# Performance work log

Measured on AMD Instinct MI355X. Metric: run time of the kernel, lower is better.

## Reference

```python
import jax, jax.numpy as jnp
import numpy as np


def setup_inputs() -> dict:
    key = jax.random.key(0)
    ks = jax.random.split(key, 10)
    N, E, F = 20000, 320000, 128
    q = jax.random.normal(ks[0], (N, F), dtype=jnp.float32)
    mu = jax.random.normal(ks[1], (N, 3, F), dtype=jnp.float32)
    W_ij = jax.random.normal(ks[2], (E, 3 * F), dtype=jnp.float32)
    dir_ij = jax.random.normal(ks[3], (E, 3), dtype=jnp.float32)
    # unit displacement vectors
    dir_ij = dir_ij / jnp.linalg.norm(dir_ij, axis=-1, keepdims=True)
    W1 = jax.random.normal(ks[4], (F, F), dtype=jnp.float32) * (1.0 / np.sqrt(F))
    b1 = jax.random.normal(ks[5], (F,), dtype=jnp.float32) * 0.01
    W2 = jax.random.normal(ks[6], (F, 3 * F), dtype=jnp.float32) * (1.0 / np.sqrt(F))
    b2 = jax.random.normal(ks[7], (3 * F,), dtype=jnp.float32) * 0.01
    idx_i = jax.random.randint(ks[8], (E,), 0, N, dtype=jnp.int64 if jax.config.jax_enable_x64 else jnp.int32)
    idx_j = jax.random.randint(ks[9], (E,), 0, N, dtype=jnp.int64 if jax.config.jax_enable_x64 else jnp.int32)
    return {"q": q, "mu": mu, "W_ij": W_ij, "dir_ij": dir_ij,
            "W1": W1, "b1": b1, "W2": W2, "b2": b2,
            "idx_i": idx_i, "idx_j": idx_j, "n_atoms": N}


def reference(q, mu, W_ij, dir_ij, W1, b1, W2, b2, idx_i, idx_j, n_atoms):
    Fdim = q.shape[-1]
    # context_net: Linear(F,F) -> SiLU -> Linear(F,3F), computed per node [N,3F]
    ctx = jax.nn.silu(q @ W1 + b1) @ W2 + b2
    # gather by source node, elementwise filter: [E,3F]
    x = W_ij * ctx[idx_j]
    dq, dmu_r, dmu_mu = jnp.split(x, 3, axis=-1)  # each [E,F]
    # scatter-add scalar messages to nodes [N,F]
    dq = jax.ops.segment_sum(dq, idx_i, num_segments=n_atoms)
    # vector messages: [E,3,F]
    dmu = dmu_r[:, None, :] * dir_ij[:, :, None] + dmu_mu[:, None, :] * mu[idx_j]
    dmu = jax.ops.segment_sum(dmu, idx_i, num_segments=n_atoms)
    return (q + dq, mu + dmu)
```

## Files before the change

kernel.cpp:

```cpp
#include <hip/hip_runtime.h>


static __host__ __device__ inline size_t ws_align(size_t x) { return (x + 255) & ~(size_t)255; }

template <bool SILU>
__global__ __launch_bounds__(256, 2) void gemm_bias_act_kernel(
    const float* __restrict__ A, const float* __restrict__ B,
    const float* __restrict__ bias, float* __restrict__ C,
    int M, int Ncols)
{
    __shared__ float As[128][68];
    __shared__ float Bs[128][68];

    const int t    = threadIdx.x;
    const int row0 = blockIdx.x * 64;
    const int col0 = blockIdx.y * 64;

    #pragma unroll
    for (int it = 0; it < 8; ++it) {
        int l    = t + 256 * it;
        int r    = l >> 5;
        int k4   = (l & 31) << 2;
        int grow = row0 + r;
        float4 v = make_float4(0.f, 0.f, 0.f, 0.f);
        if (grow < M) v = *reinterpret_cast<const float4*>(A + (size_t)grow * 128 + k4);
        As[k4 + 0][r] = v.x; As[k4 + 1][r] = v.y;
        As[k4 + 2][r] = v.z; As[k4 + 3][r] = v.w;
    }
    #pragma unroll
    for (int it = 0; it < 8; ++it) {
        int l  = t + 256 * it;
        int k  = l >> 4;
        int c4 = (l & 15) << 2;
        float4 v = *reinterpret_cast<const float4*>(B + (size_t)k * Ncols + col0 + c4);
        *reinterpret_cast<float4*>(&Bs[k][c4]) = v;
    }
    __syncthreads();

    const int tx = t & 15, ty = t >> 4;
    float acc[4][4];
    #pragma unroll
    for (int i = 0; i < 4; ++i)
        #pragma unroll
        for (int j = 0; j < 4; ++j) acc[i][j] = 0.f;

    #pragma unroll 4
    for (int k = 0; k < 128; ++k) {
        float4 a = *reinterpret_cast<const float4*>(&As[k][ty * 4]);
        float4 b = *reinterpret_cast<const float4*>(&Bs[k][tx * 4]);
        acc[0][0] += a.x * b.x; acc[0][1] += a.x * b.y; acc[0][2] += a.x * b.z; acc[0][3] += a.x * b.w;
        acc[1][0] += a.y * b.x; acc[1][1] += a.y * b.y; acc[1][2] += a.y * b.z; acc[1][3] += a.y * b.w;
        acc[2][0] += a.z * b.x; acc[2][1] += a.z * b.y; acc[2][2] += a.z * b.z; acc[2][3] += a.z * b.w;
        acc[3][0] += a.w * b.x; acc[3][1] += a.w * b.y; acc[3][2] += a.w * b.z; acc[3][3] += a.w * b.w;
    }

    float4 bv = *reinterpret_cast<const float4*>(bias + col0 + tx * 4);
    #pragma unroll
    for (int i = 0; i < 4; ++i) {
        int grow = row0 + ty * 4 + i;
        if (grow >= M) continue;
        float4 o;
        o.x = acc[i][0] + bv.x; o.y = acc[i][1] + bv.y;
        o.z = acc[i][2] + bv.z; o.w = acc[i][3] + bv.w;
        if (SILU) {
            o.x = o.x / (1.f + __expf(-o.x));
            o.y = o.y / (1.f + __expf(-o.y));
            o.z = o.z / (1.f + __expf(-o.z));
            o.w = o.w / (1.f + __expf(-o.w));
        }
        *reinterpret_cast<float4*>(C + (size_t)grow * Ncols + col0 + tx * 4) = o;
    }
}

__global__ void zero_int_kernel(int* __restrict__ p, int n) {
    int i = blockIdx.x * 256 + threadIdx.x;
    if (i < n) p[i] = 0;
}

__global__ void count_kernel(const int* __restrict__ idx_i, int* __restrict__ cnt, int E) {
    int e = blockIdx.x * 256 + threadIdx.x;
    if (e < E) atomicAdd(&cnt[idx_i[e]], 1);
}

__global__ __launch_bounds__(256) void scan_kernel(const int* __restrict__ cnt,
                                                   int* __restrict__ row_ptr, int N) {
    __shared__ int sums[256];
    __shared__ int offs[256];
    int t = threadIdx.x;
    int chunk = (N + 255) / 256;
    int lo = t * chunk;
    int hi = lo + chunk; if (hi > N) hi = N; if (lo > N) lo = N;
    int s = 0;
    for (int i = lo; i < hi; ++i) s += cnt[i];
    sums[t] = s;
    __syncthreads();
    if (t == 0) {
        int acc = 0;
        for (int k = 0; k < 256; ++k) { int v = sums[k]; offs[k] = acc; acc += v; }
    }
    __syncthreads();
    int acc = offs[t];
    for (int i = lo; i < hi; ++i) { row_ptr[i] = acc; acc += cnt[i]; }
    if (t == 255) row_ptr[N] = acc;
}

__global__ void copy_int_kernel(const int* __restrict__ src, int* __restrict__ dst, int n) {
    int i = blockIdx.x * 256 + threadIdx.x;
    if (i < n) dst[i] = src[i];
}

__global__ void fill_kernel(const int* __restrict__ idx_i, int* __restrict__ cursor,
                            int* __restrict__ order, int E) {
    int e = blockIdx.x * 256 + threadIdx.x;
    if (e < E) {
        int pos = atomicAdd(&cursor[idx_i[e]], 1);
        order[pos] = e;
    }
}

__global__ __launch_bounds__(256) void node_kernel(
    const float* __restrict__ q, const float* __restrict__ mu,
    const float* __restrict__ ctx, const float* __restrict__ W_ij,
    const float* __restrict__ dir_ij, const int* __restrict__ idx_j,
    const int* __restrict__ row_ptr, const int* __restrict__ order,
    float* __restrict__ out, int N)
{
    int wid  = (blockIdx.x * blockDim.x + threadIdx.x) >> 6;
    int lane = threadIdx.x & 63;
    if (wid >= N) return;

    int start = row_ptr[wid];
    int end   = row_ptr[wid + 1];
    const int f = lane * 2;

    float2 qa  = {0.f, 0.f};
    float2 ma0 = {0.f, 0.f}, ma1 = {0.f, 0.f}, ma2 = {0.f, 0.f};

    for (int p = start; p < end; ++p) {
        int e = order[p];
        int j = idx_j[e];
        const float* w  = W_ij + (size_t)e * 384;
        const float* cj = ctx  + (size_t)j * 384;
        const float* mj = mu   + (size_t)j * 384;
        float d0 = dir_ij[3 * (size_t)e + 0];
        float d1 = dir_ij[3 * (size_t)e + 1];
        float d2 = dir_ij[3 * (size_t)e + 2];

        float2 wq = *reinterpret_cast<const float2*>(w + f);
        float2 wr = *reinterpret_cast<const float2*>(w + 128 + f);
        float2 wm = *reinterpret_cast<const float2*>(w + 256 + f);
        float2 cq = *reinterpret_cast<const float2*>(cj + f);
        float2 cr = *reinterpret_cast<const float2*>(cj + 128 + f);
        float2 cm = *reinterpret_cast<const float2*>(cj + 256 + f);
        float2 m0 = *reinterpret_cast<const float2*>(mj + f);
        float2 m1 = *reinterpret_cast<const float2*>(mj + 128 + f);
        float2 m2 = *reinterpret_cast<const float2*>(mj + 256 + f);

        qa.x += wq.x * cq.x;  qa.y += wq.y * cq.y;
        float xr0 = wr.x * cr.x, xr1 = wr.y * cr.y;
        float xm0 = wm.x * cm.x, xm1 = wm.y * cm.y;
        ma0.x += xr0 * d0 + xm0 * m0.x;  ma0.y += xr1 * d0 + xm1 * m0.y;
        ma1.x += xr0 * d1 + xm0 * m1.x;  ma1.y += xr1 * d1 + xm1 * m1.y;
        ma2.x += xr0 * d2 + xm0 * m2.x;  ma2.y += xr1 * d2 + xm1 * m2.y;
    }

    float2 qv = *reinterpret_cast<const float2*>(q + (size_t)wid * 128 + f);
    float2 oq; oq.x = qv.x + qa.x; oq.y = qv.y + qa.y;
    *reinterpret_cast<float2*>(out + (size_t)wid * 128 + f) = oq;

    const float* mbase = mu + (size_t)wid * 384;
    float* obase = out + (size_t)N * 128 + (size_t)wid * 384;
    float2 mv0 = *reinterpret_cast<const float2*>(mbase + f);
    float2 mv1 = *reinterpret_cast<const float2*>(mbase + 128 + f);
    float2 mv2 = *reinterpret_cast<const float2*>(mbase + 256 + f);
    float2 o0; o0.x = mv0.x + ma0.x; o0.y = mv0.y + ma0.y;
    float2 o1; o1.x = mv1.x + ma1.x; o1.y = mv1.y + ma1.y;
    float2 o2; o2.x = mv2.x + ma2.x; o2.y = mv2.y + ma2.y;
    *reinterpret_cast<float2*>(obase + f)       = o0;
    *reinterpret_cast<float2*>(obase + 128 + f) = o1;
    *reinterpret_cast<float2*>(obase + 256 + f) = o2;
}

extern "C" void kernel_launch(void* const* d_in, const int* in_sizes, int n_in,
                              void* d_out, int out_size, void* d_ws, size_t ws_size,
                              hipStream_t stream) {
    const float* q      = (const float*)d_in[0];
    const float* mu     = (const float*)d_in[1];
    const float* W_ij   = (const float*)d_in[2];
    const float* dir_ij = (const float*)d_in[3];
    const float* W1     = (const float*)d_in[4];
    const float* b1     = (const float*)d_in[5];
    const float* W2     = (const float*)d_in[6];
    const float* b2     = (const float*)d_in[7];
    const int*   idx_i  = (const int*)d_in[8];
    const int*   idx_j  = (const int*)d_in[9];

    const int N = in_sizes[0] / 128;
    const int E = in_sizes[8];
    float* out = (float*)d_out;

    char* ws = (char*)d_ws;
    size_t off = 0;
    float* ctx     = (float*)(ws + off); off += ws_align((size_t)N * 384 * 4);
    float* h       = (float*)(ws + off); off += ws_align((size_t)N * 128 * 4);
    int*   row_ptr = (int*)  (ws + off); off += ws_align((size_t)(N + 1) * 4);
    int*   cursor  = (int*)  (ws + off); off += ws_align((size_t)N * 4);
    int*   order   = (int*)  (ws + off); off += ws_align((size_t)E * 4);
    (void)ws_size; (void)n_in; (void)out_size;

    const int nblk_rows = (N + 63) / 64;
    const int eblk = (E + 255) / 256;
    const int nblk = (N + 255) / 256;

    gemm_bias_act_kernel<true ><<<dim3(nblk_rows, 2), 256, 0, stream>>>(q, W1, b1, h,   N, 128);
    gemm_bias_act_kernel<false><<<dim3(nblk_rows, 6), 256, 0, stream>>>(h, W2, b2, ctx, N, 384);

    zero_int_kernel<<<nblk, 256, 0, stream>>>(cursor, N);
    count_kernel<<<eblk, 256, 0, stream>>>(idx_i, cursor, E);
    scan_kernel<<<1, 256, 0, stream>>>(cursor, row_ptr, N);
    copy_int_kernel<<<nblk, 256, 0, stream>>>(row_ptr, cursor, N);
    fill_kernel<<<eblk, 256, 0, stream>>>(idx_i, cursor, order, E);

    node_kernel<<<(N + 3) / 4, 256, 0, stream>>>(q, mu, ctx, W_ij, dir_ij, idx_j,
                                                 row_ptr, order, out, N);
}
```

Measured before the change: 904.9 us.

## Pack edge payloads, unroll gather loop by 4, use nontemporal streaming loads

The scan kernel now writes the cursor array itself, so the separate copy kernel is gone. The fill kernel stores (edge, source) pairs, which removes the dependent idx_j lookup from the node kernel. The node kernel unrolls its per-edge gather by 4 so more independent loads are in flight, and uses nontemporal loads and stores for the streamed W_ij, dir_ij and output data. In exchange it uses more registers (possibly lower occupancy) and a larger payload buffer.

```diff
diff --git a/kernel.cpp b/kernel.cpp
--- a/kernel.cpp
+++ b/kernel.cpp
@@ -1,5 +1,7 @@
 #include <hip/hip_runtime.h>
 
+
+typedef float f2 __attribute__((ext_vector_type(2)));
 
 static __host__ __device__ inline size_t ws_align(size_t x) { return (x + 255) & ~(size_t)255; }
 
@@ -82,7 +84,7 @@
     if (e < E) atomicAdd(&cnt[idx_i[e]], 1);
 }
 
-__global__ __launch_bounds__(256) void scan_kernel(const int* __restrict__ cnt,
+__global__ __launch_bounds__(256) void scan_kernel(int* __restrict__ cnt_cursor,
                                                    int* __restrict__ row_ptr, int N) {
     __shared__ int sums[256];
     __shared__ int offs[256];
@@ -91,7 +93,7 @@
     int lo = t * chunk;
     int hi = lo + chunk; if (hi > N) hi = N; if (lo > N) lo = N;
     int s = 0;
-    for (int i = lo; i < hi; ++i) s += cnt[i];
+    for (int i = lo; i < hi; ++i) s += cnt_cursor[i];
     sums[t] = s;
     __syncthreads();
     if (t == 0) {
@@ -100,85 +102,113 @@
     }
     __syncthreads();
     int acc = offs[t];
-    for (int i = lo; i < hi; ++i) { row_ptr[i] = acc; acc += cnt[i]; }
+    for (int i = lo; i < hi; ++i) {
+        int v = cnt_cursor[i];
+        cnt_cursor[i] = acc;
+        row_ptr[i]    = acc;
+        acc += v;
+    }
     if (t == 255) row_ptr[N] = acc;
 }
 
-__global__ void copy_int_kernel(const int* __restrict__ src, int* __restrict__ dst, int n) {
-    int i = blockIdx.x * 256 + threadIdx.x;
-    if (i < n) dst[i] = src[i];
-}
-
-__global__ void fill_kernel(const int* __restrict__ idx_i, int* __restrict__ cursor,
-                            int* __restrict__ order, int E) {
+__global__ void fill_kernel(const int* __restrict__ idx_i, const int* __restrict__ idx_j,
+                            int* __restrict__ cursor, int2* __restrict__ payload, int E) {
     int e = blockIdx.x * 256 + threadIdx.x;
     if (e < E) {
         int pos = atomicAdd(&cursor[idx_i[e]], 1);
-        order[pos] = e;
+        payload[pos] = make_int2(e, idx_j[e]);
     }
 }
 
 __global__ __launch_bounds__(256) void node_kernel(
     const float* __restrict__ q, const float* __restrict__ mu,
     const float* __restrict__ ctx, const float* __restrict__ W_ij,
-    const float* __restrict__ dir_ij, const int* __restrict__ idx_j,
-    const int* __restrict__ row_ptr, const int* __restrict__ order,
-    float* __restrict__ out, int N)
+    const float* __restrict__ dir_ij, const int* __restrict__ row_ptr,
+    const int2* __restrict__ payload, float* __restrict__ out, int N)
 {
     int wid  = (blockIdx.x * blockDim.x + threadIdx.x) >> 6;
     int lane = threadIdx.x & 63;
     if (wid >= N) return;
 
-    int start = row_ptr[wid];
-    int end   = row_ptr[wid + 1];
+    int p   = row_ptr[wid];
+    int end = row_ptr[wid + 1];
     const int f = lane * 2;
 
-    float2 qa  = {0.f, 0.f};
-    float2 ma0 = {0.f, 0.f}, ma1 = {0.f, 0.f}, ma2 = {0.f, 0.f};
-
-    for (int p = start; p < end; ++p) {
-        int e = order[p];
-        int j = idx_j[e];
-        const float* w  = W_ij + (size_t)e * 384;
-        const float* cj = ctx  + (size_t)j * 384;
-        const float* mj = mu   + (size_t)j * 384;
-        float d0 = dir_ij[3 * (size_t)e + 0];
-        float d1 = dir_ij[3 * (size_t)e + 1];
-        float d2 = dir_ij[3 * (size_t)e + 2];
-
-        float2 wq = *reinterpret_cast<const float2*>(w + f);
-        float2 wr = *reinterpret_cast<const float2*>(w + 128 + f);
-        float2 wm = *reinterpret_cast<const float2*>(w + 256 + f);
-        float2 cq = *reinterpret_cast<const float2*>(cj + f);
-        float2 cr = *reinterpret_cast<const float2*>(cj + 128 + f);
-        float2 cm = *reinterpret_cast<const float2*>(cj + 256 + f);
-        float2 m0 = *reinterpret_cast<const float2*>(mj + f);
-        float2 m1 = *reinterpret_cast<const float2*>(mj + 128 + f);
-        float2 m2 = *reinterpret_cast<const float2*>(mj + 256 + f);
-
-        qa.x += wq.x * cq.x;  qa.y += wq.y * cq.y;
-        float xr0 = wr.x * cr.x, xr1 = wr.y * cr.y;
-        float xm0 = wm.x * cm.x, xm1 = wm.y * cm.y;
-        ma0.x += xr0 * d0 + xm0 * m0.x;  ma0.y += xr1 * d0 + xm1 * m0.y;
-        ma1.x += xr0 * d1 + xm0 * m1.x;  ma1.y += xr1 * d1 + xm1 * m1.y;
-        ma2.x += xr0 * d2 + xm0 * m2.x;  ma2.y += xr1 * d2 + xm1 * m2.y;
-    }
-
-    float2 qv = *reinterpret_cast<const float2*>(q + (size_t)wid * 128 + f);
-    float2 oq; oq.x = qv.x + qa.x; oq.y = qv.y + qa.y;
-    *reinterpret_cast<float2*>(out + (size_t)wid * 128 + f) = oq;
+    f2 qa  = {0.f, 0.f};
+    f2 ma0 = {0.f, 0.f}, ma1 = {0.f, 0.f}, ma2 = {0.f, 0.f};
+
+    while (p + 4 <= end) {
+        int2 pl[4];
+        #pragma unroll
+        for (int u = 0; u < 4; ++u) pl[u] = payload[p + u];
+
+        f2 wq[4], wr[4], wm[4], cq[4], cr[4], cm[4], m0[4], m1[4], m2[4];
+        float d0[4], d1[4], d2[4];
+        #pragma unroll
+        for (int u = 0; u < 4; ++u) {
+            const float* w  = W_ij + (size_t)pl[u].x * 384;
+            const float* cj = ctx  + (size_t)pl[u].y * 384;
+            const float* mj = mu   + (size_t)pl[u].y * 384;
+            wq[u] = __builtin_nontemporal_load(reinterpret_cast<const f2*>(w + f));
+            wr[u] = __builtin_nontemporal_load(reinterpret_cast<const f2*>(w + 128 + f));
+            wm[u] = __builtin_nontemporal_load(reinterpret_cast<const f2*>(w + 256 + f));
+            cq[u] = *reinterpret_cast<const f2*>(cj + f);
+            cr[u] = *reinterpret_cast<const f2*>(cj + 128 + f);
+            cm[u] = *reinterpret_cast<const f2*>(cj + 256 + f);
+            m0[u] = *reinterpret_cast<const f2*>(mj + f);
+            m1[u] = *reinterpret_cast<const f2*>(mj + 128 + f);
+            m2[u] = *reinterpret_cast<const f2*>(mj + 256 + f);
+            d0[u] = __builtin_nontemporal_load(dir_ij + 3 * (size_t)pl[u].x + 0);
+            d1[u] = __builtin_nontemporal_load(dir_ij + 3 * (size_t)pl[u].x + 1);
+            d2[u] = __builtin_nontemporal_load(dir_ij + 3 * (size_t)pl[u].x + 2);
+        }
+        #pragma unroll
+        for (int u = 0; u < 4; ++u) {
+            qa += wq[u] * cq[u];
+            f2 xr = wr[u] * cr[u];
+            f2 xm = wm[u] * cm[u];
+            ma0 += xr * d0[u] + xm * m0[u];
+            ma1 += xr * d1[u] + xm * m1[u];
+            ma2 += xr * d2[u] + xm * m2[u];
+        }
+        p += 4;
+    }
+    while (p < end) {
+        int2 pl = payload[p++];
+        const float* w  = W_ij + (size_t)pl.x * 384;
+        const float* cj = ctx  + (size_t)pl.y * 384;
+        const float* mj = mu   + (size_t)pl.y * 384;
+        f2 wq = __builtin_nontemporal_load(reinterpret_cast<const f2*>(w + f));
+        f2 wr = __builtin_nontemporal_load(reinterpret_cast<const f2*>(w + 128 + f));
+        f2 wm = __builtin_nontemporal_load(reinterpret_cast<const f2*>(w + 256 + f));
+        f2 cq = *reinterpret_cast<const f2*>(cj + f);
+        f2 cr = *reinterpret_cast<const f2*>(cj + 128 + f);
+        f2 cm = *reinterpret_cast<const f2*>(cj + 256 + f);
+        f2 m0 = *reinterpret_cast<const f2*>(mj + f);
+        f2 m1 = *reinterpret_cast<const f2*>(mj + 128 + f);
+        f2 m2 = *reinterpret_cast<const f2*>(mj + 256 + f);
+        float d0 = __builtin_nontemporal_load(dir_ij + 3 * (size_t)pl.x + 0);
+        float d1 = __builtin_nontemporal_load(dir_ij + 3 * (size_t)pl.x + 1);
+        float d2 = __builtin_nontemporal_load(dir_ij + 3 * (size_t)pl.x + 2);
+        qa += wq * cq;
+        f2 xr = wr * cr;
+        f2 xm = wm * cm;
+        ma0 += xr * d0 + xm * m0;
+        ma1 += xr * d1 + xm * m1;
+        ma2 += xr * d2 + xm * m2;
+    }
+
+    f2 qv = __builtin_nontemporal_load(reinterpret_cast<const f2*>(q + (size_t)wid * 128 + f));
+    __builtin_nontemporal_store(qv + qa, reinterpret_cast<f2*>(out + (size_t)wid * 128 + f));
 
     const float* mbase = mu + (size_t)wid * 384;
     float* obase = out + (size_t)N * 128 + (size_t)wid * 384;
-    float2 mv0 = *reinterpret_cast<const float2*>(mbase + f);
-    float2 mv1 = *reinterpret_cast<const float2*>(mbase + 128 + f);
-    float2 mv2 = *reinterpret_cast<const float2*>(mbase + 256 + f);
-    float2 o0; o0.x = mv0.x + ma0.x; o0.y = mv0.y + ma0.y;
-    float2 o1; o1.x = mv1.x + ma1.x; o1.y = mv1.y + ma1.y;
-    float2 o2; o2.x = mv2.x + ma2.x; o2.y = mv2.y + ma2.y;
-    *reinterpret_cast<float2*>(obase + f)       = o0;
-    *reinterpret_cast<float2*>(obase + 128 + f) = o1;
-    *reinterpret_cast<float2*>(obase + 256 + f) = o2;
+    f2 mv0 = *reinterpret_cast<const f2*>(mbase + f);
+    f2 mv1 = *reinterpret_cast<const f2*>(mbase + 128 + f);
+    f2 mv2 = *reinterpret_cast<const f2*>(mbase + 256 + f);
+    __builtin_nontemporal_store(mv0 + ma0, reinterpret_cast<f2*>(obase + f));
+    __builtin_nontemporal_store(mv1 + ma1, reinterpret_cast<f2*>(obase + 128 + f));
+    __builtin_nontemporal_store(mv2 + ma2, reinterpret_cast<f2*>(obase + 256 + f));
 }
 
 extern "C" void kernel_launch(void* const* d_in, const int* in_sizes, int n_in,
@@ -205,7 +235,7 @@
     float* h       = (float*)(ws + off); off += ws_align((size_t)N * 128 * 4);
     int*   row_ptr = (int*)  (ws + off); off += ws_align((size_t)(N + 1) * 4);
     int*   cursor  = (int*)  (ws + off); off += ws_align((size_t)N * 4);
-    int*   order   = (int*)  (ws + off); off += ws_align((size_t)E * 4);
+    int2*  payload = (int2*) (ws + off); off += ws_align((size_t)E * 8);
     (void)ws_size; (void)n_in; (void)out_size;
 
     const int nblk_rows = (N + 63) / 64;
@@ -218,9 +248,8 @@
     zero_int_kernel<<<nblk, 256, 0, stream>>>(cursor, N);
     count_kernel<<<eblk, 256, 0, stream>>>(idx_i, cursor, E);
     scan_kernel<<<1, 256, 0, stream>>>(cursor, row_ptr, N);
-    copy_int_kernel<<<nblk, 256, 0, stream>>>(row_ptr, cursor, N);
-    fill_kernel<<<eblk, 256, 0, stream>>>(idx_i, cursor, order, E);
-
-    node_kernel<<<(N + 3) / 4, 256, 0, stream>>>(q, mu, ctx, W_ij, dir_ij, idx_j,
-                                                 row_ptr, order, out, N);
-}
+    fill_kernel<<<eblk, 256, 0, stream>>>(idx_i, idx_j, cursor, payload, E);
+
+    node_kernel<<<(N + 3) / 4, 256, 0, stream>>>(q, mu, ctx, W_ij, dir_ij,
+                                                 row_ptr, payload, out, N);
+}
```

Result: no change. 919.4 us (+1.6%).
